# Optimization experiments

Measured on AMD Instinct MI355X. Metric: run time of the kernel, lower is better.

## Reference

```python
import jax, jax.numpy as jnp
import numpy as np

BETA = 0.25

def setup_inputs() -> dict:
    key = jax.random.key(0)
    k1, k2 = jax.random.split(key)
    z_e = jax.random.normal(k1, (32, 256, 32, 32), dtype=jnp.float32)
    embed_weight = jax.random.normal(k2, (4096, 256), dtype=jnp.float32) * 0.1
    return {"z_e": z_e, "embed_weight": embed_weight}

def reference(z_e, embed_weight):
    # Eval-mode forward (no input noise, no EMA buffer update).
    B, C, H, W = z_e.shape
    K = embed_weight.shape[0]
    z_t = jnp.transpose(z_e, (0, 2, 3, 1))            # [B,H,W,C]
    z_flat = z_t.reshape(-1, C)                        # [N,C]
    # Squared Euclidean distances; argmin is identical to argmin of cdist(p=2).
    d = (
        jnp.sum(z_flat * z_flat, axis=1, keepdims=True)
        - 2.0 * (z_flat @ embed_weight.T)
        + jnp.sum(embed_weight * embed_weight, axis=1)
    )                                                  # [N,K]
    idx = jnp.argmin(d, axis=1)                        # [N]
    # utilization = (#unique codes used) / vocab_size, jit-safe via bincount-style scatter
    counts = jnp.zeros((K,), dtype=jnp.float32).at[idx].add(1.0)
    utilization = jnp.sum(counts > 0).astype(jnp.float32) / K
    z_q = embed_weight[idx].reshape(B, H, W, C)        # [B,H,W,C]
    commitment_loss = jnp.mean((jax.lax.stop_gradient(z_q) - z_t) ** 2) * BETA
    z_q_st = z_t + jax.lax.stop_gradient(z_q - z_t)    # straight-through
    return jnp.transpose(z_q_st, (0, 3, 1, 2)), commitment_loss, utilization
```

## Files before the change

### kernel.cpp

```cpp
#include <hip/hip_runtime.h>
#include <math.h>


#define WGAP 52

using half8 = __attribute__((ext_vector_type(8))) _Float16;
using f32x4 = __attribute__((ext_vector_type(4))) float;

__device__ __forceinline__ void gload_lds16(const void* g, void* l) {
  __builtin_amdgcn_global_load_lds(
      (const __attribute__((address_space(1))) unsigned int*)g,
      (__attribute__((address_space(3))) unsigned int*)l, 16, 0, 0);
}

__device__ __forceinline__ bool lexlt64(double v, int x, double ov, int ox) {
  return (v < ov) || (v == ov && x < ox);
}

__device__ __forceinline__ int med3i(int a, int b, int c) {
  int d;
  asm("v_med3_i32 %0, %1, %2, %3" : "=v"(d) : "v"(a), "v"(b), "v"(c));
  return d;
}

__device__ __forceinline__ void ins3k(int key, int& a0, int& a1, int& a2) {
  const int n2 = min(a2, max(key, a1));
  const int n1 = med3i(key, a0, a1);
  a0 = min(key, a0);
  a1 = n1;
  a2 = n2;
}

__device__ __forceinline__ void mrg3k(int& a0, int& a1, int& a2,
                                      int b0, int b1, int b2) {
  const int c0 = min(a0, b0);
  const int x = max(a0, b0);
  const int y = min(a1, b1);
  const int c1 = min(x, y);
  const int z = max(x, y);
  const int ww = min(a2, b2);
  const int c2 = min(z, ww);
  a0 = c0; a1 = c1; a2 = c2;
}

__global__ __launch_bounds__(256) void vq_prep(const float* __restrict__ E,
                                               uint4* __restrict__ Epk,
                                               float* __restrict__ en1024,
                                               int* __restrict__ used,
                                               double* __restrict__ lossSum,
                                               int* __restrict__ candCount,
                                               int* __restrict__ messyCount) {
  const int t = blockIdx.x * 256 + threadIdx.x;
  if (t < 4096) used[t] = 0;
  if (t == 4096) *lossSum = 0.0;
  if (t == 4097) *candCount = 0;
  if (t == 4098) *messyCount = 0;
  const int code = t >> 5, j = t & 31;
  const int rc = code & 63;
  const float* src = E + (size_t)code * 256 + j * 8;
  const float4 v0 = *(const float4*)(src);
  const float4 v1 = *(const float4*)(src + 4);
  float zv[8] = {v0.x, v0.y, v0.z, v0.w, v1.x, v1.y, v1.z, v1.w};
  union { half8 h; uint4 u; } pk;
  float s = 0.f;
#pragma unroll
  for (int e = 0; e < 8; ++e) {
    const float z = zv[e];
    s = fmaf(z, z, s);
    pk.h[e] = (_Float16)(z * -256.0f);
  }
  const size_t g = (size_t)((code >> 6) * 8 + (j >> 2)) * 256 +
                   rc * 4 + ((j & 3) ^ (rc & 3));
  Epk[g] = pk.u;
#pragma unroll
  for (int off = 1; off < 32; off <<= 1) s += __shfl_xor(s, off);
  if (j == 0) en1024[code] = s * 1024.0f;
}

__global__ __launch_bounds__(256, 3) void vq_screen(
    const float* __restrict__ Z, const char* __restrict__ Epk,
    const float* __restrict__ en1024,
    int* __restrict__ pk0, int* __restrict__ pk1, int* __restrict__ pk2) {
  __shared__ char lds[49152];
  const int tid = threadIdx.x;
  const int w = tid >> 6, l = tid & 63;
  const int xcd = blockIdx.x & 7, inner = blockIdx.x >> 3;
  const int part = inner % 3;
  const int qg = (inner / 3) * 8 + xcd;
  const int chs = part * 21 + (part > 0 ? 1 : 0);
  const int che = chs + (part == 0 ? 22 : 21);
  const int S = (che - chs) * 8;
  const int qbase = qg * 128;
  const int b = qbase >> 10;
  const int hwq = (qbase & 1023) + w * 32 + (l & 15);

  char* myLds = lds + w * 12288;
  const char* EpkBase = Epk + ((size_t)(chs * 8) << 12) + l * 16;

  auto stage = [&](int q, int slot) {
    const char* src = EpkBase + ((size_t)q << 12);
    char* dst = myLds + slot * 4096;
#pragma unroll
    for (int i = 0; i < 4; ++i) gload_lds16(src + i * 1024, dst + i * 1024);
  };
  stage(0, 0);
  stage(1, 1);

  const float* Zq = Z + (size_t)b * 262144 + hwq;
  half8 ah[2][8];
#pragma unroll
  for (int u = 0; u < 2; ++u)
#pragma unroll
    for (int ks = 0; ks < 8; ++ks) {
      const int c0 = ks * 32 + (l >> 4) * 8;
#pragma unroll
      for (int e = 0; e < 8; ++e)
        ah[u][ks][e] = (_Float16)(Zq[u * 16 + ((size_t)(c0 + e) << 10)] * 8.0f);
    }

  const int lo0 = (l & 15) * 64 + (((l >> 4) ^ (l & 3)) << 4);

  int k0[2][4], k1[2][4], k2[2][4];
#pragma unroll
  for (int u = 0; u < 2; ++u)
#pragma unroll
    for (int r = 0; r < 4; ++r) {
      k0[u][r] = 0x7fffffff; k1[u][r] = 0x7fffffff; k2[u][r] = 0x7fffffff;
    }

  int cur = 0, pf = 2, q = 0;
  for (int ch = chs; ch < che; ++ch) {
    const int cb = ch * 64;
    f32x4 acc[2][4];
#pragma unroll
    for (int t = 0; t < 4; ++t) {
      const float en = en1024[cb + t * 16 + (l & 15)];
      acc[0][t] = (f32x4){en, en, en, en};
      acc[1][t] = (f32x4){en, en, en, en};
    }

#pragma unroll
    for (int ks = 0; ks < 8; ++ks) {
      if (q + 2 < S) {
        stage(q + 2, pf);
        asm volatile("s_waitcnt vmcnt(8)" ::: "memory");
      } else {
        asm volatile("s_waitcnt vmcnt(0)" ::: "memory");
      }
      const char* Lb = myLds + cur * 4096;
      __builtin_amdgcn_s_setprio(1);
#pragma unroll
      for (int t = 0; t < 4; ++t) {
        const half8 eh = *(const half8*)(Lb + lo0 + t * 1024);
        acc[0][t] = __builtin_amdgcn_mfma_f32_16x16x32_f16(ah[0][ks], eh, acc[0][t], 0, 0, 0);
        acc[1][t] = __builtin_amdgcn_mfma_f32_16x16x32_f16(ah[1][ks], eh, acc[1][t], 0, 0, 0);
      }
      __builtin_amdgcn_s_setprio(0);
      cur = (cur == 2) ? 0 : cur + 1;
      pf = (pf == 2) ? 0 : pf + 1;
      ++q;
    }

#pragma unroll
    for (int t = 0; t < 4; ++t) {
      const int code = cb + t * 16 + (l & 15);
#pragma unroll
      for (int u = 0; u < 2; ++u)
#pragma unroll
        for (int r = 0; r < 4; ++r) {
          const int di = (int)acc[u][t][r];
          const int key = (int)(((unsigned)di << 12) + (unsigned)code);
          ins3k(key, k0[u][r], k1[u][r], k2[u][r]);
        }
    }
  }

#pragma unroll
  for (int mask = 1; mask <= 8; mask <<= 1) {
#pragma unroll
    for (int u = 0; u < 2; ++u)
#pragma unroll
      for (int r = 0; r < 4; ++r) {
        const int o0 = __shfl_xor(k0[u][r], mask);
        const int o1 = __shfl_xor(k1[u][r], mask);
        const int o2 = __shfl_xor(k2[u][r], mask);
        mrg3k(k0[u][r], k1[u][r], k2[u][r], o0, o1, o2);
      }
  }
  if ((l & 15) == 0) {
#pragma unroll
    for (int u = 0; u < 2; ++u)
#pragma unroll
      for (int r = 0; r < 4; ++r) {
        const int n = qbase + w * 32 + u * 16 + (l >> 4) * 4 + r;
        const int o = part * 32768 + n;
        pk0[o] = k0[u][r]; pk1[o] = k1[u][r]; pk2[o] = k2[u][r];
      }
  }
}

__global__ __launch_bounds__(256) void vq_merge(
    const int* __restrict__ pk0, const int* __restrict__ pk1,
    const int* __restrict__ pk2, int* __restrict__ idxOut,
    int* __restrict__ cand, int* __restrict__ candCount,
    int* __restrict__ messy, int* __restrict__ messyCount,
    int* __restrict__ pi0, int* __restrict__ pi1, int* __restrict__ pi2) {
  const int n = blockIdx.x * 256 + threadIdx.x;
  int a0 = pk0[n], a1 = pk1[n], a2 = pk2[n];
#pragma unroll
  for (int q = 1; q < 3; ++q) {
    const int o = q * 32768 + n;
    mrg3k(a0, a1, a2, pk0[o], pk1[o], pk2[o]);
  }
  const int x0 = a0 & 0xfff;
  idxOut[n] = x0;
  const int d0 = a0 >> 12, d1 = a1 >> 12, d2 = a2 >> 12;
  if (d1 - d0 < WGAP) {
    if (d2 - d0 < WGAP) {
      const int p = atomicAdd(messyCount, 1);
      if (p < 4096) messy[p] = n;
    } else {
      const int p = atomicAdd(candCount, 1);
      cand[p] = n;
      pi0[n] = x0; pi1[n] = a1 & 0xfff; pi2[n] = a2 & 0xfff;
    }
  }
}

__global__ __launch_bounds__(256) void vq_exact(
    const float* __restrict__ Z, const float* __restrict__ E,
    const int* __restrict__ pi0, const int* __restrict__ pi1,
    const int* __restrict__ pi2, const int* __restrict__ cand,
    const int* __restrict__ candCount, const int* __restrict__ messy,
    const int* __restrict__ messyCount, double* __restrict__ parv,
    int* __restrict__ parx, int* __restrict__ idxOut) {
  __shared__ float zs[4][256];
  __shared__ double rv[4][256];
  __shared__ int ri[4][256];
  const int t = threadIdx.x;
  const int w = t >> 6, l = t & 63;

  if (blockIdx.x < 256) {
    const int cnt = *candCount;
    for (int j = blockIdx.x * 4 + w; j < cnt; j += 1024) {
      const int n = cand[j];
      const int b = n >> 10, hw = n & 1023;
      const int ca = pi0[n], cbn = pi1[n], cc = pi2[n];
      float z4[4];
#pragma unroll
      for (int i = 0; i < 4; ++i)
        z4[i] = Z[(size_t)b * 262144 + ((size_t)(l * 4 + i) << 10) + hw];
      const float4 e0 = *(const float4*)(E + (size_t)ca * 256 + l * 4);
      const float4 e1 = *(const float4*)(E + (size_t)cbn * 256 + l * 4);
      const float4 e2 = *(const float4*)(E + (size_t)cc * 256 + l * 4);
      double d0 = 0, d1 = 0, d2 = 0;
      const float* p0 = (const float*)&e0;
      const float* p1 = (const float*)&e1;
      const float* p2 = (const float*)&e2;
#pragma unroll
      for (int i = 0; i < 4; ++i) {
        const double f0 = (double)z4[i] - (double)p0[i];
        const double f1 = (double)z4[i] - (double)p1[i];
        const double f2 = (double)z4[i] - (double)p2[i];
        d0 = fma(f0, f0, d0);
        d1 = fma(f1, f1, d1);
        d2 = fma(f2, f2, d2);
      }
#pragma unroll
      for (int off = 32; off > 0; off >>= 1) {
        d0 += __shfl_down(d0, off);
        d1 += __shfl_down(d1, off);
        d2 += __shfl_down(d2, off);
      }
      if (l == 0) {
        double bv = d0; int bx = ca;
        if (lexlt64(d1, cbn, bv, bx)) { bv = d1; bx = cbn; }
        if (lexlt64(d2, cc, bv, bx)) { bv = d2; bx = cc; }
        idxOut[n] = bx;
      }
    }
    return;
  }

  const int cnt0 = *messyCount;
  const int cnt = cnt0 > 4096 ? 4096 : cnt0;
  const int jobs = ((cnt + 3) >> 2) * 16;
  for (int job = blockIdx.x - 256; job < jobs; job += 512) {
    const int grp = job >> 4, chunk = job & 15;
    __syncthreads();
    {
      const int q = t >> 6, lq = t & 63;
      const int mi = grp * 4 + q;
      const int n = messy[mi < cnt ? mi : grp * 4];
      const int b = n >> 10, hw = n & 1023;
#pragma unroll
      for (int i = 0; i < 4; ++i)
        zs[q][lq * 4 + i] =
            Z[(size_t)b * 262144 + ((size_t)(lq * 4 + i) << 10) + hw];
    }
    __syncthreads();
    const int code = chunk * 256 + t;
    const float* er = E + (size_t)code * 256;
    double s0 = 0, s1 = 0, s2 = 0, s3 = 0;
    for (int c = 0; c < 256; ++c) {
      const double ec = (double)er[c];
      const double f0 = (double)zs[0][c] - ec;
      const double f1 = (double)zs[1][c] - ec;
      const double f2 = (double)zs[2][c] - ec;
      const double f3 = (double)zs[3][c] - ec;
      s0 = fma(f0, f0, s0);
      s1 = fma(f1, f1, s1);
      s2 = fma(f2, f2, s2);
      s3 = fma(f3, f3, s3);
    }
    rv[0][t] = s0; rv[1][t] = s1; rv[2][t] = s2; rv[3][t] = s3;
    ri[0][t] = code; ri[1][t] = code; ri[2][t] = code; ri[3][t] = code;
    __syncthreads();
    for (int s = 128; s > 0; s >>= 1) {
      if (t < s) {
#pragma unroll
        for (int qq = 0; qq < 4; ++qq)
          if (lexlt64(rv[qq][t + s], ri[qq][t + s], rv[qq][t], ri[qq][t])) {
            rv[qq][t] = rv[qq][t + s];
            ri[qq][t] = ri[qq][t + s];
          }
      }
      __syncthreads();
    }
    if (t == 0) {
#pragma unroll
      for (int qq = 0; qq < 4; ++qq) {
        const int mi = grp * 4 + qq;
        if (mi < cnt) {
          parv[mi * 16 + chunk] = rv[qq][0];
          parx[mi * 16 + chunk] = ri[qq][0];
        }
      }
    }
  }
}

__global__ __launch_bounds__(256) void vq_messy2(
    const int* __restrict__ messy, const int* __restrict__ messyCount,
    const double* __restrict__ parv, const int* __restrict__ parx,
    int* __restrict__ idxOut) {
  const int cnt0 = *messyCount;
  const int cnt = cnt0 > 4096 ? 4096 : cnt0;
  for (int j = blockIdx.x * 256 + threadIdx.x; j < cnt; j += gridDim.x * 256) {
    double bv = parv[j * 16];
    int bx = parx[j * 16];
    for (int ch = 1; ch < 16; ++ch) {
      const double v = parv[j * 16 + ch];
      const int x = parx[j * 16 + ch];
      if (lexlt64(v, x, bv, bx)) { bv = v; bx = x; }
    }
    idxOut[messy[j]] = bx;
  }
}

__global__ __launch_bounds__(256) void vq_out(
    const float* __restrict__ Z, const float* __restrict__ E,
    const int* __restrict__ idx, float* __restrict__ out,
    double* __restrict__ lossSum, int* __restrict__ used) {
  __shared__ float zt[32][257];
  __shared__ int ids[32];
  const int tid = threadIdx.x;
  const int qb = blockIdx.x * 32;
  const int b = qb >> 10, hw0 = qb & 1023;
  if (tid < 32) {
    const int id = idx[qb + tid];
    ids[tid] = id;
    used[id] = 1;
  }
  __syncthreads();
  const int w = tid >> 6, l = tid & 63;
#pragma unroll
  for (int rr = 0; rr < 8; ++rr) {
    const int q = rr * 4 + w;
    const float4 v = *(const float4*)(E + (size_t)ids[q] * 256 + l * 4);
    zt[q][l * 4 + 0] = v.x;
    zt[q][l * 4 + 1] = v.y;
    zt[q][l * 4 + 2] = v.z;
    zt[q][l * 4 + 3] = v.w;
  }
  __syncthreads();
  const int h4 = (tid & 7) * 4;
  const int c0 = tid >> 3;
  float ls = 0.f;
#pragma unroll
  for (int p = 0; p < 8; ++p) {
    const int c = p * 32 + c0;
    const size_t g = (size_t)b * 262144 + ((size_t)c << 10) + hw0 + h4;
    const float4 z4 = *(const float4*)(Z + g);
    float4 o;
    o.x = zt[h4 + 0][c];
    o.y = zt[h4 + 1][c];
    o.z = zt[h4 + 2][c];
    o.w = zt[h4 + 3][c];
    *(float4*)(out + g) = o;
    const float dx = o.x - z4.x, dy = o.y - z4.y;
    const float dz = o.z - z4.z, dw = o.w - z4.w;
    ls = fmaf(dx, dx, ls);
    ls = fmaf(dy, dy, ls);
    ls = fmaf(dz, dz, ls);
    ls = fmaf(dw, dw, ls);
  }
#pragma unroll
  for (int off = 32; off > 0; off >>= 1) ls += __shfl_down(ls, off);
  __shared__ float red[4];
  if (l == 0) red[w] = ls;
  __syncthreads();
  if (tid == 0)
    atomicAdd(lossSum, (double)((red[0] + red[1]) + (red[2] + red[3])));
}

__global__ __launch_bounds__(256) void vq_final(const int* __restrict__ used,
                                                const double* __restrict__ lossSum,
                                                float* __restrict__ out) {
  __shared__ int cnt[256];
  int c = 0;
  for (int k = threadIdx.x; k < 4096; k += 256) c += (used[k] > 0);
  cnt[threadIdx.x] = c;
  __syncthreads();
  if (threadIdx.x == 0) {
    int tot = 0;
    for (int t = 0; t < 256; ++t) tot += cnt[t];
    out[8388608] = (float)(*lossSum * 0.25 / 8388608.0);
    out[8388609] = (float)tot / 4096.0f;
  }
}

extern "C" void kernel_launch(void* const* d_in, const int* in_sizes, int n_in,
                              void* d_out, int out_size, void* d_ws, size_t ws_size,
                              hipStream_t stream) {
  const float* Z = (const float*)d_in[0];
  const float* E = (const float*)d_in[1];
  float* out = (float*)d_out;
  char* w = (char*)d_ws;

  int* idx = (int*)w;
  int* cand = (int*)(w + 131072);
  float* en1024 = (float*)(w + 262144);
  int* used = (int*)(w + 278528);
  double* lossSum = (double*)(w + 294912);
  int* candCount = (int*)(w + 294920);
  int* messyCount = (int*)(w + 294924);

  char* Epk16 = (char*)out;
  int* pk0 = (int*)(out + 524288);
  int* pk1 = (int*)(out + 655360);
  int* pk2 = (int*)(out + 786432);
  int* pi0 = (int*)(out + 917504);
  int* pi1 = (int*)(out + 950272);
  int* pi2 = (int*)(out + 983040);
  int* messy = (int*)(out + 1015808);
  double* parv = (double*)(out + 1019904);
  int* parx = (int*)(out + 1150976);

  vq_prep<<<512, 256, 0, stream>>>(E, (uint4*)Epk16, en1024, used, lossSum,
                                   candCount, messyCount);
  vq_screen<<<768, 256, 0, stream>>>(Z, Epk16, en1024, pk0, pk1, pk2);
  vq_merge<<<128, 256, 0, stream>>>(pk0, pk1, pk2, idx, cand, candCount,
                                    messy, messyCount, pi0, pi1, pi2);
  vq_exact<<<768, 256, 0, stream>>>(Z, E, pi0, pi1, pi2, cand, candCount,
                                    messy, messyCount, parv, parx, idx);
  vq_messy2<<<8, 256, 0, stream>>>(messy, messyCount, parv, parx, idx);
  vq_out<<<1024, 256, 0, stream>>>(Z, E, idx, out, lossSum, used);
  vq_final<<<1, 256, 0, stream>>>(used, lossSum, out);
}
```

Measured before the change: 182.6 us.

## Read codebook tiles directly from global memory instead of LDS triple-buffering

Removes the per-wave LDS triple-buffered staging of packed codebook fragments via global_load_lds and instead loads the B-operand fragments directly from global memory into registers for the MFMAs. The packed codebook layout in the prep kernel changes to match, with each lane reading contiguous 16-byte pieces. This drops the LDS footprint and the waitcnt pipeline, which may allow higher occupancy. In exchange, MFMAs now depend on global or L2 latency with no explicit prefetch, relying on occupancy and the compiler to hide it.

```diff
diff --git a/kernel.cpp b/kernel.cpp
--- a/kernel.cpp
+++ b/kernel.cpp
@@ -6,12 +6,6 @@
 
 using half8 = __attribute__((ext_vector_type(8))) _Float16;
 using f32x4 = __attribute__((ext_vector_type(4))) float;
-
-__device__ __forceinline__ void gload_lds16(const void* g, void* l) {
-  __builtin_amdgcn_global_load_lds(
-      (const __attribute__((address_space(1))) unsigned int*)g,
-      (__attribute__((address_space(3))) unsigned int*)l, 16, 0, 0);
-}
 
 __device__ __forceinline__ bool lexlt64(double v, int x, double ov, int ox) {
   return (v < ov) || (v == ov && x < ox);
@@ -56,7 +50,6 @@
   if (t == 4097) *candCount = 0;
   if (t == 4098) *messyCount = 0;
   const int code = t >> 5, j = t & 31;
-  const int rc = code & 63;
   const float* src = E + (size_t)code * 256 + j * 8;
   const float4 v0 = *(const float4*)(src);
   const float4 v1 = *(const float4*)(src + 4);
@@ -69,8 +62,7 @@
     s = fmaf(z, z, s);
     pk.h[e] = (_Float16)(z * -256.0f);
   }
-  const size_t g = (size_t)((code >> 6) * 8 + (j >> 2)) * 256 +
-                   rc * 4 + ((j & 3) ^ (rc & 3));
+  const size_t g = (size_t)(code >> 6) * 2048 + j * 64 + (code & 63);
   Epk[g] = pk.u;
 #pragma unroll
   for (int off = 1; off < 32; off <<= 1) s += __shfl_xor(s, off);
@@ -81,7 +73,6 @@
     const float* __restrict__ Z, const char* __restrict__ Epk,
     const float* __restrict__ en1024,
     int* __restrict__ pk0, int* __restrict__ pk1, int* __restrict__ pk2) {
-  __shared__ char lds[49152];
   const int tid = threadIdx.x;
   const int w = tid >> 6, l = tid & 63;
   const int xcd = blockIdx.x & 7, inner = blockIdx.x >> 3;
@@ -89,23 +80,10 @@
   const int qg = (inner / 3) * 8 + xcd;
   const int chs = part * 21 + (part > 0 ? 1 : 0);
   const int che = chs + (part == 0 ? 22 : 21);
-  const int S = (che - chs) * 8;
   const int qbase = qg * 128;
   const int b = qbase >> 10;
   const int hwq = (qbase & 1023) + w * 32 + (l & 15);
 
-  char* myLds = lds + w * 12288;
-  const char* EpkBase = Epk + ((size_t)(chs * 8) << 12) + l * 16;
-
-  auto stage = [&](int q, int slot) {
-    const char* src = EpkBase + ((size_t)q << 12);
-    char* dst = myLds + slot * 4096;
-#pragma unroll
-    for (int i = 0; i < 4; ++i) gload_lds16(src + i * 1024, dst + i * 1024);
-  };
-  stage(0, 0);
-  stage(1, 1);
-
   const float* Zq = Z + (size_t)b * 262144 + hwq;
   half8 ah[2][8];
 #pragma unroll
@@ -118,7 +96,7 @@
         ah[u][ks][e] = (_Float16)(Zq[u * 16 + ((size_t)(c0 + e) << 10)] * 8.0f);
     }
 
-  const int lo0 = (l & 15) * 64 + (((l >> 4) ^ (l & 3)) << 4);
+  const char* Eb = Epk + (l >> 4) * 1024 + (l & 15) * 16;
 
   int k0[2][4], k1[2][4], k2[2][4];
 #pragma unroll
@@ -128,9 +106,9 @@
       k0[u][r] = 0x7fffffff; k1[u][r] = 0x7fffffff; k2[u][r] = 0x7fffffff;
     }
 
-  int cur = 0, pf = 2, q = 0;
   for (int ch = chs; ch < che; ++ch) {
     const int cb = ch * 64;
+    const char* Cb = Eb + (size_t)ch * 32768;
     f32x4 acc[2][4];
 #pragma unroll
     for (int t = 0; t < 4; ++t) {
@@ -139,27 +117,24 @@
       acc[1][t] = (f32x4){en, en, en, en};
     }
 
+    __builtin_amdgcn_s_setprio(1);
 #pragma unroll
     for (int ks = 0; ks < 8; ++ks) {
-      if (q + 2 < S) {
-        stage(q + 2, pf);
-        asm volatile("s_waitcnt vmcnt(8)" ::: "memory");
-      } else {
-        asm volatile("s_waitcnt vmcnt(0)" ::: "memory");
-      }
-      const char* Lb = myLds + cur * 4096;
-      __builtin_amdgcn_s_setprio(1);
-#pragma unroll
-      for (int t = 0; t < 4; ++t) {
-        const half8 eh = *(const half8*)(Lb + lo0 + t * 1024);
-        acc[0][t] = __builtin_amdgcn_mfma_f32_16x16x32_f16(ah[0][ks], eh, acc[0][t], 0, 0, 0);
-        acc[1][t] = __builtin_amdgcn_mfma_f32_16x16x32_f16(ah[1][ks], eh, acc[1][t], 0, 0, 0);
-      }
-      __builtin_amdgcn_s_setprio(0);
-      cur = (cur == 2) ? 0 : cur + 1;
-      pf = (pf == 2) ? 0 : pf + 1;
-      ++q;
-    }
+      const char* p = Cb + ks * 4096;
+      const half8 e0 = *(const half8*)(p);
+      const half8 e1 = *(const half8*)(p + 256);
+      const half8 e2 = *(const half8*)(p + 512);
+      const half8 e3 = *(const half8*)(p + 768);
+      acc[0][0] = __builtin_amdgcn_mfma_f32_16x16x32_f16(ah[0][ks], e0, acc[0][0], 0, 0, 0);
+      acc[1][0] = __builtin_amdgcn_mfma_f32_16x16x32_f16(ah[1][ks], e0, acc[1][0], 0, 0, 0);
+      acc[0][1] = __builtin_amdgcn_mfma_f32_16x16x32_f16(ah[0][ks], e1, acc[0][1], 0, 0, 0);
+      acc[1][1] = __builtin_amdgcn_mfma_f32_16x16x32_f16(ah[1][ks], e1, acc[1][1], 0, 0, 0);
+      acc[0][2] = __builtin_amdgcn_mfma_f32_16x16x32_f16(ah[0][ks], e2, acc[0][2], 0, 0, 0);
+      acc[1][2] = __builtin_amdgcn_mfma_f32_16x16x32_f16(ah[1][ks], e2, acc[1][2], 0, 0, 0);
+      acc[0][3] = __builtin_amdgcn_mfma_f32_16x16x32_f16(ah[0][ks], e3, acc[0][3], 0, 0, 0);
+      acc[1][3] = __builtin_amdgcn_mfma_f32_16x16x32_f16(ah[1][ks], e3, acc[1][3], 0, 0, 0);
+    }
+    __builtin_amdgcn_s_setprio(0);
 
 #pragma unroll
     for (int t = 0; t < 4; ++t) {
```

Result: no change. 185.9 us (+1.8%).
